# Kernel optimization log

Measured on AMD Instinct MI355X. Metric: run time of the kernel, lower is better.

## Reference

```python
import jax, jax.numpy as jnp
import numpy as np

D_MODEL = 768
N_HEADS = 12
D_K = D_MODEL // N_HEADS
NEG = -1e9


def setup_inputs() -> dict:
    key = jax.random.key(0)
    ks = jax.random.split(key, 10)
    B, S = 2, 2048
    x = jax.random.normal(ks[0], (B, S, D_MODEL), dtype=jnp.float32)
    # causal mask, broadcastable over batch and heads
    mask = jnp.tril(jnp.ones((S, S), dtype=jnp.int32))[None, None]
    scale = 1.0 / np.sqrt(D_MODEL)
    def lin(k):
        return jax.random.normal(k, (D_MODEL, D_MODEL), dtype=jnp.float32) * scale
    return {
        "x": x, "mask": mask,
        "wq": lin(ks[1]), "bq": jnp.zeros((D_MODEL,), jnp.float32),
        "wk": lin(ks[2]), "bk": jnp.zeros((D_MODEL,), jnp.float32),
        "wv": lin(ks[3]), "bv": jnp.zeros((D_MODEL,), jnp.float32),
        "wo": lin(ks[4]), "bo": jnp.zeros((D_MODEL,), jnp.float32),
    }


def reference(x, mask, wq, bq, wk, bk, wv, bv, wo, bo):
    B, S, _ = x.shape
    def split_heads(t):  # [B,S,D] -> [B,H,S,dk]
        return t.reshape(B, S, N_HEADS, D_K).transpose(0, 2, 1, 3)
    q = split_heads(x @ wq + bq)
    k = split_heads(x @ wk + bk)
    v = split_heads(x @ wv + bv)
    scores = jnp.einsum("bhqd,bhkd->bhqk", q, k) / jnp.sqrt(jnp.float32(D_K))
    scores = jnp.where(mask == 0, NEG, scores)
    attn = jax.nn.softmax(scores, axis=-1)
    # dropout is identity in eval mode
    ctx = jnp.einsum("bhqk,bhkd->bhqd", attn, v)
    ctx = ctx.transpose(0, 2, 1, 3).reshape(B, S, D_MODEL)
    return ctx @ wo + bo
```

## Files before the change

kernel.cpp:

```cpp
#include <hip/hip_runtime.h>
#include <hip/hip_bf16.h>
#include <stdint.h>

#define DM   768
#define NH   12
#define DKH  64
#define BB   2
#define SS   2048
#define MT   (BB*SS)
#define NQKV (3*DM)

typedef __attribute__((ext_vector_type(8))) short short8;
typedef __attribute__((ext_vector_type(4))) float f32x4;

__device__ __forceinline__ unsigned short f2bf(float f) {
    union { float f; unsigned u; } v; v.f = f;
    unsigned r = v.u + 0x7fffu + ((v.u >> 16) & 1u);
    return (unsigned short)(r >> 16);
}

__device__ __forceinline__ void gload_lds16(const unsigned short* g, unsigned short* l) {
    __builtin_amdgcn_global_load_lds((const __attribute__((address_space(1))) void*)g,
                                     (__attribute__((address_space(3))) void*)l, 16, 0, 0);
}

__launch_bounds__(256)
__global__ void k_conv(const float* __restrict__ x, unsigned short* __restrict__ xb,
                       const float* __restrict__ wq, const float* __restrict__ wk,
                       const float* __restrict__ wv, const float* __restrict__ wo,
                       unsigned short* __restrict__ wT) {
    __shared__ float tile[32][33];
    const int t = threadIdx.x;
    if (blockIdx.x < 3072) {
        int i = blockIdx.x * 256 + t;
        const float4 v = ((const float4*)x)[i];
        ushort4 o;
        o.x = f2bf(v.x); o.y = f2bf(v.y); o.z = f2bf(v.z); o.w = f2bf(v.w);
        ((ushort4*)xb)[i] = o;
    } else {
        const int cid = blockIdx.x - 3072;
        const int sel = cid / 576;
        const int rem = cid - sel * 576;
        const int kb = rem / 24, nb = rem - (rem / 24) * 24;
        const float* w = (sel == 0) ? wq : (sel == 1) ? wk : (sel == 2) ? wv : wo;
        const int k0 = kb * 32, n0 = nb * 32;
        const int tx = t & 31, ty = t >> 5;
        #pragma unroll
        for (int j = 0; j < 4; j++)
            tile[ty + 8*j][tx] = w[(size_t)(k0 + ty + 8*j) * DM + n0 + tx];
        __syncthreads();
        #pragma unroll
        for (int j = 0; j < 4; j++)
            wT[(size_t)(sel*DM + n0 + ty + 8*j) * DM + k0 + tx] = f2bf(tile[tx][ty + 8*j]);
    }
}

__launch_bounds__(256)
__global__ void k_gemm_qkv(const unsigned short* __restrict__ xb,
                           const unsigned short* __restrict__ wT,
                           const float* __restrict__ bq, const float* __restrict__ bk,
                           const float* __restrict__ bv,
                           unsigned short* __restrict__ Qb,
                           unsigned short* __restrict__ Kb,
                           unsigned short* __restrict__ Vt) {
    __shared__ __align__(16) unsigned short As[128][32];
    __shared__ __align__(16) unsigned short Bs[128][32];
    const int t = threadIdx.x;
    const int m0 = blockIdx.x * 128;
    const int n0 = blockIdx.y * 128;
    const int wid = t >> 6, lane = t & 63, q4 = lane >> 4, l16 = lane & 15;
    const int wm = (wid >> 1) * 64, wn = (wid & 1) * 64;

    const int srow = wid * 32 + (lane >> 2);
    const int koff = (lane & 3) * 8;
    const unsigned short* AgL = xb + (size_t)(m0 + srow) * DM + koff;
    const unsigned short* AgH = AgL + (size_t)16 * DM;
    const unsigned short* BgL = wT + (size_t)(n0 + srow) * DM + koff;
    const unsigned short* BgH = BgL + (size_t)16 * DM;
    unsigned short* ldsA1 = &As[wid*32][0];
    unsigned short* ldsA2 = &As[wid*32 + 16][0];
    unsigned short* ldsB1 = &Bs[wid*32][0];
    unsigned short* ldsB2 = &Bs[wid*32 + 16][0];

    f32x4 acc[4][4];
    for (int i = 0; i < 4; i++) for (int j = 0; j < 4; j++)
        acc[i][j] = (f32x4){0.f, 0.f, 0.f, 0.f};

    for (int kt = 0; kt < DM; kt += 32) {
        gload_lds16(AgL + kt, ldsA1);
        gload_lds16(AgH + kt, ldsA2);
        gload_lds16(BgL + kt, ldsB1);
        gload_lds16(BgH + kt, ldsB2);
        __syncthreads();
        short8 af[4], bf[4];
        for (int i = 0; i < 4; i++) af[i] = *(const short8*)&As[wm + i*16 + l16][q4*8];
        for (int i = 0; i < 4; i++) bf[i] = *(const short8*)&Bs[wn + i*16 + l16][q4*8];
        for (int mi = 0; mi < 4; mi++)
            for (int ni = 0; ni < 4; ni++)
                acc[mi][ni] = __builtin_amdgcn_mfma_f32_16x16x32_bf16(af[mi], bf[ni], acc[mi][ni], 0, 0, 0);
        __syncthreads();
    }

    const int sel = n0 / DM;
    const float* bias = (sel == 0) ? bq : (sel == 1) ? bk : bv;
    for (int ni = 0; ni < 4; ni++) {
        const int col = n0 + wn + ni*16 + l16;
        const int c = col - sel * DM;
        const float bsv = bias[c];
        const int h = c >> 6, d = c & 63;
        for (int mi = 0; mi < 4; mi++) {
            for (int r = 0; r < 4; r++) {
                const int row = m0 + wm + mi*16 + q4*4 + r;
                const int b = row >> 11, s = row & 2047;
                const int bh = b * NH + h;
                float v = acc[mi][ni][r] + bsv;
                if (sel == 0) {
                    Qb[(bh*SS + s)*DKH + d] = f2bf(v * 0.125f);
                } else if (sel == 1) {
                    Kb[(bh*SS + s)*DKH + d] = f2bf(v);
                } else {
                    Vt[(bh*DKH + d)*SS + s] = f2bf(v);
                }
            }
        }
    }
}

__device__ const int UNITS[48] = {
  (15<<16)|(0<<8)|16, (31<<16)|(0<<8)|16, (31<<16)|(16<<8)|32, (30<<16)|(0<<8)|16,
  (14<<16)|(0<<8)|15, (29<<16)|(0<<8)|15, (29<<16)|(15<<8)|30, (28<<16)|(0<<8)|15, (30<<16)|(16<<8)|31,
  (13<<16)|(0<<8)|14, (27<<16)|(0<<8)|14, (27<<16)|(14<<8)|28, (26<<16)|(0<<8)|14, (28<<16)|(15<<8)|29,
  (12<<16)|(0<<8)|13, (25<<16)|(0<<8)|13, (25<<16)|(13<<8)|26, (24<<16)|(0<<8)|13, (26<<16)|(14<<8)|27,
  (11<<16)|(0<<8)|12, (23<<16)|(0<<8)|12, (23<<16)|(12<<8)|24, (22<<16)|(0<<8)|12, (24<<16)|(13<<8)|25,
  (10<<16)|(0<<8)|11, (21<<16)|(0<<8)|11, (21<<16)|(11<<8)|22, (20<<16)|(0<<8)|11, (22<<16)|(12<<8)|23,
  ( 9<<16)|(0<<8)|10, (19<<16)|(0<<8)|10, (19<<16)|(10<<8)|20, (18<<16)|(0<<8)|10, (20<<16)|(11<<8)|21,
  ( 8<<16)|(0<<8)| 9, (17<<16)|(0<<8)| 9, (17<<16)|( 9<<8)|18, (16<<16)|(0<<8)| 9, (18<<16)|(10<<8)|19,
  ( 7<<16)|(0<<8)| 8, (16<<16)|( 9<<8)|17,
  ( 6<<16)|(0<<8)| 7, ( 5<<16)|(0<<8)| 6, ( 4<<16)|(0<<8)| 5, ( 3<<16)|(0<<8)| 4,
  ( 2<<16)|(0<<8)| 3, ( 1<<16)|(0<<8)| 2, ( 0<<16)|(0<<8)| 1,
};

__launch_bounds__(256, 4)
__global__ void k_attn(const unsigned short* __restrict__ Qb,
                       const unsigned short* __restrict__ Kb,
                       const unsigned short* __restrict__ Vt,
                       unsigned short* __restrict__ ctx,
                       float* __restrict__ Opart, float* __restrict__ lpart) {
    __shared__ __align__(16) unsigned short Ks[2][64*64];
    __shared__ __align__(16) unsigned short Vs[2][64*64];
    __shared__ __align__(16) unsigned short P2[4][16*64];
    const int t = threadIdx.x;
    const int wid = t >> 6, lane = t & 63, q4 = lane >> 4, l16 = lane & 15;

    const int lin = blockIdx.x;
    const int bh = lin % 24;
    const int info = UNITS[lin / 24];
    const int qblk = info >> 16, t0 = (info >> 8) & 0xff, t1 = info & 0xff;
    const int b = bh / NH, h = bh - b * NH;
    const int qw = qblk * 64 + wid * 16;

    const unsigned short* Qp = Qb + (size_t)bh * SS * DKH;
    const unsigned short* Kp = Kb + (size_t)bh * SS * DKH;
    const unsigned short* Vp = Vt + (size_t)bh * DKH * SS;

    const int sr  = t >> 3;
    const int sc8 = (t & 7) * 8;
    const int scs = sc8 ^ ((sr & 7) * 8);
    const int swz = (l16 & 7) * 8;

    short8 qf[2];
    qf[0] = *(const short8*)(Qp + (size_t)(qw + l16)*DKH +      q4*8);
    qf[1] = *(const short8*)(Qp + (size_t)(qw + l16)*DKH + 32 + q4*8);

    f32x4 accO[4];
    #pragma unroll
    for (int j = 0; j < 4; j++) accO[j] = (f32x4){0.f, 0.f, 0.f, 0.f};
    float lacc = 0.f;

    {
        const int kb0 = t0 * 64;
        *(uint4*)&Ks[0][ sr    *64 + scs] = *(const uint4*)(Kp + (size_t)(kb0 + sr)     *DKH + sc8);
        *(uint4*)&Ks[0][(sr+32)*64 + scs] = *(const uint4*)(Kp + (size_t)(kb0 + sr + 32)*DKH + sc8);
        *(uint4*)&Vs[0][ sr    *64 + scs] = *(const uint4*)(Vp + (size_t) sr     *SS + kb0 + sc8);
        *(uint4*)&Vs[0][(sr+32)*64 + scs] = *(const uint4*)(Vp + (size_t)(sr+32) *SS + kb0 + sc8);
    }
    __syncthreads();

    for (int kt = t0; kt < t1; kt++) {
        const int cb = (kt - t0) & 1, nb = cb ^ 1;
        const bool hasN = (kt + 1 < t1);
        uint4 nk0, nk1, nv0, nv1;
        if (hasN) {
            const int kn = (kt + 1) * 64;
            nk0 = *(const uint4*)(Kp + (size_t)(kn + sr)      * DKH + sc8);
            nk1 = *(const uint4*)(Kp + (size_t)(kn + sr + 32) * DKH + sc8);
            nv0 = *(const uint4*)(Vp + (size_t)(sr)      * SS + kn + sc8);
            nv1 = *(const uint4*)(Vp + (size_t)(sr + 32) * SS + kn + sc8);
        }
        f32x4 St[4];
        #pragma unroll
        for (int ni = 0; ni < 4; ni++) St[ni] = (f32x4){0.f, 0.f, 0.f, 0.f};
        __builtin_amdgcn_s_setprio(1);
        #pragma unroll
        for (int ni = 0; ni < 4; ni++) {
            const int rbase = (ni*16 + l16) * 64;
            short8 kf0 = *(const short8*)&Ks[cb][rbase + ((     q4*8) ^ swz)];
            short8 kf1 = *(const short8*)&Ks[cb][rbase + ((32 + q4*8) ^ swz)];
            St[ni] = __builtin_amdgcn_mfma_f32_16x16x32_bf16(kf0, qf[0], St[ni], 0, 0, 0);
            St[ni] = __builtin_amdgcn_mfma_f32_16x16x32_bf16(kf1, qf[1], St[ni], 0, 0, 0);
        }
        __builtin_amdgcn_s_setprio(0);
        if (kt < qblk) {
            #pragma unroll
            for (int ni = 0; ni < 4; ni++) {
                float p0 = __expf(St[ni][0]), p1 = __expf(St[ni][1]);
                float p2 = __expf(St[ni][2]), p3 = __expf(St[ni][3]);
                lacc += (p0 + p1) + (p2 + p3);
                union { __hip_bfloat162 v; unsigned u; } u01, u23;
                u01.v = __float22bfloat162_rn(make_float2(p0, p1));
                u23.v = __float22bfloat162_rn(make_float2(p2, p3));
                uint2 pk; pk.x = u01.u; pk.y = u23.u;
                *(uint2*)&P2[wid][l16*64 + ((ni*16 + q4*4) ^ swz)] = pk;
            }
        } else {
            const int qrow = qw + l16;
            #pragma unroll
            for (int ni = 0; ni < 4; ni++) {
                const int key0 = kt*64 + ni*16 + q4*4;
                float p[4];
                #pragma unroll
                for (int r = 0; r < 4; r++) {
                    p[r] = (key0 + r > qrow) ? 0.f : __expf(St[ni][r]);
                    lacc += p[r];
                }
                union { __hip_bfloat162 v; unsigned u; } u01, u23;
                u01.v = __float22bfloat162_rn(make_float2(p[0], p[1]));
                u23.v = __float22bfloat162_rn(make_float2(p[2], p[3]));
                uint2 pk; pk.x = u01.u; pk.y = u23.u;
                *(uint2*)&P2[wid][l16*64 + ((ni*16 + q4*4) ^ swz)] = pk;
            }
        }
        asm volatile("s_waitcnt lgkmcnt(0)" ::: "memory");
        short8 pf[2];
        pf[0] = *(const short8*)&P2[wid][l16*64 + ((     q4*8) ^ swz)];
        pf[1] = *(const short8*)&P2[wid][l16*64 + ((32 + q4*8) ^ swz)];
        __builtin_amdgcn_s_setprio(1);
        #pragma unroll
        for (int ndi = 0; ndi < 4; ndi++) {
            const int rbase = (ndi*16 + l16) * 64;
            short8 vf0 = *(const short8*)&Vs[cb][rbase + ((     q4*8) ^ swz)];
            short8 vf1 = *(const short8*)&Vs[cb][rbase + ((32 + q4*8) ^ swz)];
            accO[ndi] = __builtin_amdgcn_mfma_f32_16x16x32_bf16(vf0, pf[0], accO[ndi], 0, 0, 0);
            accO[ndi] = __builtin_amdgcn_mfma_f32_16x16x32_bf16(vf1, pf[1], accO[ndi], 0, 0, 0);
        }
        __builtin_amdgcn_s_setprio(0);
        if (hasN) {
            *(uint4*)&Ks[nb][ sr    *64 + scs] = nk0;
            *(uint4*)&Ks[nb][(sr+32)*64 + scs] = nk1;
            *(uint4*)&Vs[nb][ sr    *64 + scs] = nv0;
            *(uint4*)&Vs[nb][(sr+32)*64 + scs] = nv1;
        }
        __syncthreads();
    }

    float l = lacc;
    l += __shfl_xor(l, 16);
    l += __shfl_xor(l, 32);

    if (qblk < 16) {
        const float inv = 1.0f / l;
        const size_t row = (size_t)(b*SS + qw + l16);
        #pragma unroll
        for (int ndi = 0; ndi < 4; ndi++) {
            ushort4 o;
            o.x = f2bf(accO[ndi][0] * inv);
            o.y = f2bf(accO[ndi][1] * inv);
            o.z = f2bf(accO[ndi][2] * inv);
            o.w = f2bf(accO[ndi][3] * inv);
            *(ushort4*)&ctx[row*DM + h*64 + ndi*16 + q4*4] = o;
        }
    } else {
        const int pair  = bh * 16 + (qblk - 16);
        const int chunk = (t0 != 0);
        const int qloc  = wid * 16 + l16;
        float* Op = Opart + ((size_t)pair * 2 + chunk) * 4096;
        #pragma unroll
        for (int ndi = 0; ndi < 4; ndi++)
            *(f32x4*)&Op[qloc*64 + ndi*16 + q4*4] = accO[ndi];
        if (q4 == 0) lpart[pair*128 + chunk*64 + qloc] = l;
    }
}

__launch_bounds__(256)
__global__ void k_combine(const float* __restrict__ Opart,
                          const float* __restrict__ lpart,
                          unsigned short* __restrict__ ctx) {
    const int pair = blockIdx.x;
    const int bh = pair >> 4, qblk = 16 + (pair & 15);
    const int b = bh / NH, h = bh - b * NH;
    const int t = threadIdx.x;
    const int q = t >> 2, dg = (t & 3) * 16;
    const float* P0 = Opart + (size_t)pair * 2 * 4096;
    const float* P1 = P0 + 4096;
    const float* L0 = lpart + pair * 128;
    const float inv = 1.0f / (L0[q] + L0[64 + q]);
    const size_t row = (size_t)(b*SS + qblk*64 + q);
    #pragma unroll
    for (int i = 0; i < 4; i++) {
        f32x4 a = *(const f32x4*)&P0[q*64 + dg + i*4];
        f32x4 c = *(const f32x4*)&P1[q*64 + dg + i*4];
        ushort4 o;
        o.x = f2bf((a[0] + c[0]) * inv);
        o.y = f2bf((a[1] + c[1]) * inv);
        o.z = f2bf((a[2] + c[2]) * inv);
        o.w = f2bf((a[3] + c[3]) * inv);
        *(ushort4*)&ctx[row*DM + h*64 + dg + i*4] = o;
    }
}

__launch_bounds__(256)
__global__ void k_gemm_proj(const unsigned short* __restrict__ ctx,
                            const unsigned short* __restrict__ woT,
                            const float* __restrict__ bo,
                            float* __restrict__ out) {
    __shared__ __align__(16) unsigned short As[128][32];
    __shared__ __align__(16) unsigned short Bs[64][32];
    const int t = threadIdx.x;
    const int m0 = blockIdx.x * 128;
    const int n0 = blockIdx.y * 64;
    const int wid = t >> 6, lane = t & 63, q4 = lane >> 4, l16 = lane & 15;
    const int wm = (wid >> 1) * 64, wn = (wid & 1) * 32;

    const int srowA = wid * 32 + (lane >> 2);
    const int srowB = wid * 16 + (lane >> 2);
    const int koff = (lane & 3) * 8;
    const unsigned short* AgL = ctx + (size_t)(m0 + srowA) * DM + koff;
    const unsigned short* AgH = AgL + (size_t)16 * DM;
    const unsigned short* BgL = woT + (size_t)(n0 + srowB) * DM + koff;
    unsigned short* ldsA1 = &As[wid*32][0];
    unsigned short* ldsA2 = &As[wid*32 + 16][0];
    unsigned short* ldsB1 = &Bs[wid*16][0];

    f32x4 acc[4][2];
    for (int i = 0; i < 4; i++) for (int j = 0; j < 2; j++)
        acc[i][j] = (f32x4){0.f, 0.f, 0.f, 0.f};

    for (int kt = 0; kt < DM; kt += 32) {
        gload_lds16(AgL + kt, ldsA1);
        gload_lds16(AgH + kt, ldsA2);
        gload_lds16(BgL + kt, ldsB1);
        __syncthreads();
        short8 af[4], bf[2];
        for (int i = 0; i < 4; i++) af[i] = *(const short8*)&As[wm + i*16 + l16][q4*8];
        for (int i = 0; i < 2; i++) bf[i] = *(const short8*)&Bs[wn + i*16 + l16][q4*8];
        for (int mi = 0; mi < 4; mi++)
            for (int ni = 0; ni < 2; ni++)
                acc[mi][ni] = __builtin_amdgcn_mfma_f32_16x16x32_bf16(af[mi], bf[ni], acc[mi][ni], 0, 0, 0);
        __syncthreads();
    }

    for (int ni = 0; ni < 2; ni++) {
        const int col = n0 + wn + ni*16 + l16;
        const float bsv = bo[col];
        for (int mi = 0; mi < 4; mi++) {
            for (int r = 0; r < 4; r++) {
                const int row = m0 + wm + mi*16 + q4*4 + r;
                out[(size_t)row * DM + col] = acc[mi][ni][r] + bsv;
            }
        }
    }
}

extern "C" void kernel_launch(void* const* d_in, const int* in_sizes, int n_in,
                              void* d_out, int out_size, void* d_ws, size_t ws_size,
                              hipStream_t stream) {
    const float* x  = (const float*)d_in[0];
    const float* wq = (const float*)d_in[2];
    const float* bq = (const float*)d_in[3];
    const float* wk = (const float*)d_in[4];
    const float* bk = (const float*)d_in[5];
    const float* wv = (const float*)d_in[6];
    const float* bv = (const float*)d_in[7];
    const float* wo = (const float*)d_in[8];
    const float* bo = (const float*)d_in[9];
    float* out = (float*)d_out;

    unsigned short* xb  = (unsigned short*)d_ws;
    unsigned short* wT  = xb + (size_t)MT * DM;
    unsigned short* Qb  = wT + (size_t)4 * DM * DM;
    unsigned short* Kb  = Qb + (size_t)BB * NH * SS * DKH;
    unsigned short* Vt  = Kb + (size_t)BB * NH * SS * DKH;
    unsigned short* ctx = Vt + (size_t)BB * NH * SS * DKH;
    float* Opart = (float*)(ctx + (size_t)MT * DM);
    float* lpart = Opart + (size_t)768 * 4096;

    k_conv<<<3072 + 2304, 256, 0, stream>>>(x, xb, wq, wk, wv, wo, wT);
    dim3 g1(MT / 128, NQKV / 128);
    k_gemm_qkv<<<g1, 256, 0, stream>>>(xb, wT, bq, bk, bv, Qb, Kb, Vt);
    k_attn<<<dim3(1152), 256, 0, stream>>>(Qb, Kb, Vt, ctx, Opart, lpart);
    k_combine<<<dim3(384), 256, 0, stream>>>(Opart, lpart, ctx);
    dim3 g3(MT / 128, DM / 64);
    k_gemm_proj<<<g3, 256, 0, stream>>>(ctx, wT + (size_t)3 * DM * DM, bo, out);
}
```

Baseline: 168.7 us.

## Retile QKV GEMM to 128x64 tiles with K=64 steps and swizzled LDS

Changes the QKV projection GEMM from 128x128 output tiles with K-step 32 to 128x64 tiles with K-step 64, which doubles the grid to 32x36 blocks. LDS rows are XOR-swizzled to avoid bank conflicts, and the loops are fully unrolled. launch_bounds now requests 4 blocks per CU. The aim is more blocks for occupancy and fewer barriers per K, at the cost of more redundant A-tile loads.

```diff
diff --git a/kernel.cpp b/kernel.cpp
--- a/kernel.cpp
+++ b/kernel.cpp
@@ -55,7 +55,7 @@
     }
 }
 
-__launch_bounds__(256)
+__launch_bounds__(256, 4)
 __global__ void k_gemm_qkv(const unsigned short* __restrict__ xb,
                            const unsigned short* __restrict__ wT,
                            const float* __restrict__ bq, const float* __restrict__ bk,
@@ -63,47 +63,55 @@
                            unsigned short* __restrict__ Qb,
                            unsigned short* __restrict__ Kb,
                            unsigned short* __restrict__ Vt) {
-    __shared__ __align__(16) unsigned short As[128][32];
-    __shared__ __align__(16) unsigned short Bs[128][32];
+    __shared__ __align__(16) unsigned short As[128*64];
+    __shared__ __align__(16) unsigned short Bs[64*64];
     const int t = threadIdx.x;
     const int m0 = blockIdx.x * 128;
-    const int n0 = blockIdx.y * 128;
+    const int n0 = blockIdx.y * 64;
     const int wid = t >> 6, lane = t & 63, q4 = lane >> 4, l16 = lane & 15;
-    const int wm = (wid >> 1) * 64, wn = (wid & 1) * 64;
-
-    const int srow = wid * 32 + (lane >> 2);
-    const int koff = (lane & 3) * 8;
-    const unsigned short* AgL = xb + (size_t)(m0 + srow) * DM + koff;
-    const unsigned short* AgH = AgL + (size_t)16 * DM;
-    const unsigned short* BgL = wT + (size_t)(n0 + srow) * DM + koff;
-    const unsigned short* BgH = BgL + (size_t)16 * DM;
-    unsigned short* ldsA1 = &As[wid*32][0];
-    unsigned short* ldsA2 = &As[wid*32 + 16][0];
-    unsigned short* ldsB1 = &Bs[wid*32][0];
-    unsigned short* ldsB2 = &Bs[wid*32 + 16][0];
-
-    f32x4 acc[4][4];
-    for (int i = 0; i < 4; i++) for (int j = 0; j < 4; j++)
+    const int wm = (wid >> 1) * 64, wn = (wid & 1) * 32;
+
+    const int srow = lane >> 3;
+    const int scol = ((lane & 7) ^ srow) * 8;
+    const unsigned short* Ag = xb + (size_t)(m0 + wid*8 + srow) * DM + scol;
+    const unsigned short* Bg = wT + (size_t)(n0 + wid*8 + srow) * DM + scol;
+    unsigned short* ldsA = &As[(wid*8)*64];
+    unsigned short* ldsB = &Bs[(wid*8)*64];
+    const int swz = (l16 & 7) * 8;
+
+    f32x4 acc[4][2];
+    for (int i = 0; i < 4; i++) for (int j = 0; j < 2; j++)
         acc[i][j] = (f32x4){0.f, 0.f, 0.f, 0.f};
 
-    for (int kt = 0; kt < DM; kt += 32) {
-        gload_lds16(AgL + kt, ldsA1);
-        gload_lds16(AgH + kt, ldsA2);
-        gload_lds16(BgL + kt, ldsB1);
-        gload_lds16(BgH + kt, ldsB2);
-        __syncthreads();
-        short8 af[4], bf[4];
-        for (int i = 0; i < 4; i++) af[i] = *(const short8*)&As[wm + i*16 + l16][q4*8];
-        for (int i = 0; i < 4; i++) bf[i] = *(const short8*)&Bs[wn + i*16 + l16][q4*8];
-        for (int mi = 0; mi < 4; mi++)
-            for (int ni = 0; ni < 4; ni++)
-                acc[mi][ni] = __builtin_amdgcn_mfma_f32_16x16x32_bf16(af[mi], bf[ni], acc[mi][ni], 0, 0, 0);
+    for (int kt = 0; kt < DM; kt += 64) {
+        #pragma unroll
+        for (int j = 0; j < 4; j++)
+            gload_lds16(Ag + (size_t)(j*32) * DM + kt, ldsA + j*32*64);
+        #pragma unroll
+        for (int j = 0; j < 2; j++)
+            gload_lds16(Bg + (size_t)(j*32) * DM + kt, ldsB + j*32*64);
+        __syncthreads();
+        #pragma unroll
+        for (int kc = 0; kc < 2; kc++) {
+            short8 af[4], bf[2];
+            #pragma unroll
+            for (int i = 0; i < 4; i++)
+                af[i] = *(const short8*)&As[(wm + i*16 + l16)*64 + ((kc*32 + q4*8) ^ swz)];
+            #pragma unroll
+            for (int i = 0; i < 2; i++)
+                bf[i] = *(const short8*)&Bs[(wn + i*16 + l16)*64 + ((kc*32 + q4*8) ^ swz)];
+            #pragma unroll
+            for (int mi = 0; mi < 4; mi++)
+                #pragma unroll
+                for (int ni = 0; ni < 2; ni++)
+                    acc[mi][ni] = __builtin_amdgcn_mfma_f32_16x16x32_bf16(af[mi], bf[ni], acc[mi][ni], 0, 0, 0);
+        }
         __syncthreads();
     }
 
     const int sel = n0 / DM;
     const float* bias = (sel == 0) ? bq : (sel == 1) ? bk : bv;
-    for (int ni = 0; ni < 4; ni++) {
+    for (int ni = 0; ni < 2; ni++) {
         const int col = n0 + wn + ni*16 + l16;
         const int c = col - sel * DM;
         const float bsv = bias[c];
@@ -395,7 +403,7 @@
     float* lpart = Opart + (size_t)768 * 4096;
 
     k_conv<<<3072 + 2304, 256, 0, stream>>>(x, xb, wq, wk, wv, wo, wT);
-    dim3 g1(MT / 128, NQKV / 128);
+    dim3 g1(MT / 128, NQKV / 64);
     k_gemm_qkv<<<g1, 256, 0, stream>>>(xb, wT, bq, bk, bv, Qb, Kb, Vt);
     k_attn<<<dim3(1152), 256, 0, stream>>>(Qb, Kb, Vt, ctx, Opart, lpart);
     k_combine<<<dim3(384), 256, 0, stream>>>(Opart, lpart, ctx);
```

Result: no change. 170.7 us (+1.2%).
